# Kernel tuning notes

Measured on AMD Instinct MI355X. Metric: run time of the kernel, lower is better.

## Reference

```python
import jax, jax.numpy as jnp
import numpy as np

N_NODES = 30000
N_EDGES = 150000
N_REL = 10
IN_DIM = 256
OUT_DIM = 256


def setup_inputs() -> dict:
    key = jax.random.key(0)
    ks = jax.random.split(key, 10)
    s = 1.0 / np.sqrt(IN_DIM)  # ~nn.Linear init scale
    return {
        "x": jax.random.normal(ks[0], (N_NODES, IN_DIM), jnp.float32),
        "W_self": jax.random.uniform(ks[1], (IN_DIM, OUT_DIM), jnp.float32, -s, s),
        "b_self": jax.random.uniform(ks[2], (OUT_DIM,), jnp.float32, -s, s),
        "W_fwd": jax.random.uniform(ks[3], (N_REL, IN_DIM, OUT_DIM), jnp.float32, -s, s),
        "b_fwd": jax.random.uniform(ks[4], (N_REL, OUT_DIM), jnp.float32, -s, s),
        "W_rev": jax.random.uniform(ks[5], (N_REL, IN_DIM, OUT_DIM), jnp.float32, -s, s),
        "b_rev": jax.random.uniform(ks[6], (N_REL, OUT_DIM), jnp.float32, -s, s),
        "dep_idx": jax.random.randint(ks[7], (N_EDGES,), 0, N_NODES, jnp.int32),
        "rel_idx": jax.random.randint(ks[8], (N_EDGES,), 0, N_REL, jnp.int32),
        "gov_idx": jax.random.randint(ks[9], (N_EDGES,), 0, N_NODES, jnp.int32),
    }


def reference(x, W_self, b_self, W_fwd, b_fwd, W_rev, b_rev, dep_idx, rel_idx, gov_idx):
    # self transform for every token: [N, out]
    out = x @ W_self + b_self
    # transform all nodes by every relation weight up-front: [R, N, out]
    H_fwd = jnp.einsum("ni,rio->rno", x, W_fwd) + b_fwd[:, None, :]
    H_rev = jnp.einsum("ni,rio->rno", x, W_rev) + b_rev[:, None, :]
    # per-edge gather: forward msg uses governor feature, reverse msg uses dependent
    msg_fwd = H_fwd[rel_idx, gov_idx]  # [E, out]
    msg_rev = H_rev[rel_idx, dep_idx]  # [E, out]
    # scatter-add: forward msg -> dependent, reverse msg -> governor
    out = out.at[dep_idx].add(msg_fwd)
    out = out.at[gov_idx].add(msg_rev)
    return out
```

## Files before the change

### kernel.cpp

```cpp
#include <hip/hip_runtime.h>

#define N_NODES 30000
#define N_EDGES 150000
#define N_REL 10
#define DIM 256

#define SORT_BLOCKS 120
#define SORT_CHUNK ((N_EDGES + SORT_BLOCKS - 1) / SORT_BLOCKS)

#define SCAN_CHUNK 256
#define SCAN_BLOCKS ((N_NODES + SCAN_CHUNK - 1) / SCAN_CHUNK)

#define A_STRIDE 280

typedef __attribute__((ext_vector_type(8))) short bf16x8;
typedef __attribute__((ext_vector_type(4))) float f32x4;

__device__ __forceinline__ unsigned short f2bf(float f) {
  union { float f; unsigned int u; } v; v.f = f;
  unsigned int u = v.u;
  unsigned int r = u + 0x7fffu + ((u >> 16) & 1u);
  return (unsigned short)(r >> 16);
}


__global__ void conv_x_kernel(const float* __restrict__ x,
                              unsigned short* __restrict__ xbf) {
  int idx = blockIdx.x * blockDim.x + threadIdx.x;
  float4 v = reinterpret_cast<const float4*>(x)[idx];
  ushort4 o;
  o.x = f2bf(v.x); o.y = f2bf(v.y); o.z = f2bf(v.z); o.w = f2bf(v.w);
  reinterpret_cast<ushort4*>(xbf)[idx] = o;
}

__global__ void conv_w_kernel(const float* __restrict__ Wf,
                              const float* __restrict__ Wr,
                              const float* __restrict__ Ws,
                              unsigned short* __restrict__ wt) {
  int idx = blockIdx.x * blockDim.x + threadIdx.x;
  int b = idx >> 16;
  int t = idx & 65535;
  int o = t >> 8, i = t & 255;
  const float* src = (b < N_REL) ? (Wf + (size_t)b * 65536)
                   : (b < 2 * N_REL) ? (Wr + (size_t)(b - N_REL) * 65536)
                   : Ws;
  wt[idx] = f2bf(src[i * 256 + o]);
}

__global__ void zero_cnt_kernel(int* __restrict__ cnt, int n) {
  int i = blockIdx.x * blockDim.x + threadIdx.x;
  if (i < n) cnt[i] = 0;
}

__global__ void hist_all_kernel(const int* __restrict__ rel,
                                const int* __restrict__ dep,
                                const int* __restrict__ gov,
                                int* __restrict__ block_counts,
                                int* __restrict__ cnt) {
  __shared__ int h[N_REL];
  if (threadIdx.x < N_REL) h[threadIdx.x] = 0;
  __syncthreads();
  int beg = blockIdx.x * SORT_CHUNK;
  int end = min(beg + SORT_CHUNK, N_EDGES);
  for (int e = beg + threadIdx.x; e < end; e += blockDim.x) {
    atomicAdd(&h[rel[e]], 1);
    atomicAdd(&cnt[dep[e]], 1);
    atomicAdd(&cnt[N_NODES + gov[e]], 1);
  }
  __syncthreads();
  if (threadIdx.x < N_REL)
    block_counts[blockIdx.x * N_REL + threadIdx.x] = h[threadIdx.x];
}

__global__ void scan_rel_kernel(const int* __restrict__ block_counts,
                                int* __restrict__ rel_start,
                                int* __restrict__ block_offset) {
  __shared__ int tot[N_REL];
  int r = threadIdx.x;
  if (r < N_REL) {
    int s = 0;
    for (int b = 0; b < SORT_BLOCKS; ++b) s += block_counts[b * N_REL + r];
    tot[r] = s;
  }
  __syncthreads();
  if (threadIdx.x == 0) {
    int s = 0;
    for (int i = 0; i < N_REL; ++i) { rel_start[i] = s; s += tot[i]; }
    rel_start[N_REL] = s;
  }
  __syncthreads();
  if (r < N_REL) {
    int run = rel_start[r];
    for (int b = 0; b < SORT_BLOCKS; ++b) {
      block_offset[b * N_REL + r] = run;
      run += block_counts[b * N_REL + r];
    }
  }
}

__global__ void scanA_kernel(const int* __restrict__ cnt,
                             int* __restrict__ tmp, int* __restrict__ sums) {
  __shared__ int s[SCAN_CHUNK];
  int d = blockIdx.y, b = blockIdx.x, t = threadIdx.x;
  int i = b * SCAN_CHUNK + t;
  int v = (i < N_NODES) ? cnt[d * N_NODES + i] : 0;
  s[t] = v;
  __syncthreads();
  for (int off = 1; off < SCAN_CHUNK; off <<= 1) {
    int add = (t >= off) ? s[t - off] : 0;
    __syncthreads();
    s[t] += add;
    __syncthreads();
  }
  if (i < N_NODES) tmp[d * N_NODES + i] = s[t] - v;
  if (t == SCAN_CHUNK - 1) sums[d * SCAN_BLOCKS + b] = s[t];
}

__global__ void scanB_kernel(const int* __restrict__ sums,
                             int* __restrict__ chunk_off, int* __restrict__ rp) {
  __shared__ int s[128];
  int d = blockIdx.x, t = threadIdx.x;
  int v = (t < SCAN_BLOCKS) ? sums[d * SCAN_BLOCKS + t] : 0;
  s[t] = v;
  __syncthreads();
  for (int off = 1; off < 128; off <<= 1) {
    int add = (t >= off) ? s[t - off] : 0;
    __syncthreads();
    s[t] += add;
    __syncthreads();
  }
  if (t < SCAN_BLOCKS) chunk_off[d * SCAN_BLOCKS + t] = s[t] - v;
  if (t == 127) rp[d * (N_NODES + 1) + N_NODES] = s[127];
}

__global__ void scanC_kernel(const int* __restrict__ tmp,
                             const int* __restrict__ chunk_off,
                             int* __restrict__ rp, int* __restrict__ cursor) {
  int d = blockIdx.y;
  int i = blockIdx.x * SCAN_CHUNK + threadIdx.x;
  if (i < N_NODES) {
    int v = tmp[d * N_NODES + i] + chunk_off[d * SCAN_BLOCKS + blockIdx.x];
    rp[d * (N_NODES + 1) + i] = v;
    cursor[d * N_NODES + i] = v;
  }
}

__global__ void scatter_all_kernel(const int* __restrict__ rel,
                                   const int* __restrict__ dep,
                                   const int* __restrict__ gov,
                                   const int* __restrict__ block_offset,
                                   int* __restrict__ cursor,
                                   int* __restrict__ perm,
                                   int* __restrict__ colf,
                                   int* __restrict__ colr) {
  __shared__ int cur[N_REL];
  if (threadIdx.x < N_REL)
    cur[threadIdx.x] = block_offset[blockIdx.x * N_REL + threadIdx.x];
  __syncthreads();
  int beg = blockIdx.x * SORT_CHUNK;
  int end = min(beg + SORT_CHUNK, N_EDGES);
  for (int e = beg + threadIdx.x; e < end; e += blockDim.x) {
    int pos = atomicAdd(&cur[rel[e]], 1);
    perm[pos] = e;
    colf[atomicAdd(&cursor[dep[e]], 1)] = pos;
    colr[atomicAdd(&cursor[N_NODES + gov[e]], 1)] = pos;
  }
}


__global__ __launch_bounds__(256, 2)
void self_gemm_kernel(const unsigned short* __restrict__ xbf,
                      const unsigned short* __restrict__ wt_self,
                      const float* __restrict__ b_self,
                      float* __restrict__ out) {
  const int tid = threadIdx.x;
  const int wave = tid >> 6, lane = tid & 63;
  const int lm = lane & 15, q = lane >> 4;
  const int nb = wave * 64;

  bf16x8 wf[8][4];
  #pragma unroll
  for (int kk = 0; kk < 8; ++kk)
    #pragma unroll
    for (int ni = 0; ni < 4; ++ni)
      wf[kk][ni] = *reinterpret_cast<const bf16x8*>(
          wt_self + (size_t)(nb + ni * 16 + lm) * DIM + kk * 32 + q * 8);

  float bias[4];
  #pragma unroll
  for (int ni = 0; ni < 4; ++ni) bias[ni] = b_self[nb + ni * 16 + lm];

  const int ntiles = (N_NODES + 63) / 64;
  for (int t = blockIdx.x; t < ntiles; t += gridDim.x) {
    const int row0 = t * 64;
    const unsigned short* xr[4];
    #pragma unroll
    for (int mi = 0; mi < 4; ++mi) {
      int r = row0 + mi * 16 + lm;
      int rc = r < N_NODES ? r : N_NODES - 1;
      xr[mi] = xbf + (size_t)rc * DIM + q * 8;
    }

    f32x4 acc[4][4];
    #pragma unroll
    for (int mi = 0; mi < 4; ++mi)
      #pragma unroll
      for (int ni = 0; ni < 4; ++ni)
        acc[mi][ni] = (f32x4){0.f, 0.f, 0.f, 0.f};

    #pragma unroll
    for (int kk = 0; kk < 8; ++kk) {
      bf16x8 a[4];
      #pragma unroll
      for (int mi = 0; mi < 4; ++mi)
        a[mi] = *reinterpret_cast<const bf16x8*>(xr[mi] + kk * 32);
      #pragma unroll
      for (int mi = 0; mi < 4; ++mi)
        #pragma unroll
        for (int ni = 0; ni < 4; ++ni)
          acc[mi][ni] = __builtin_amdgcn_mfma_f32_16x16x32_bf16(a[mi], wf[kk][ni], acc[mi][ni], 0, 0, 0);
    }

    #pragma unroll
    for (int mi = 0; mi < 4; ++mi) {
      #pragma unroll
      for (int reg = 0; reg < 4; ++reg) {
        int row = row0 + mi * 16 + q * 4 + reg;
        if (row < N_NODES) {
          #pragma unroll
          for (int ni = 0; ni < 4; ++ni)
            out[(size_t)row * DIM + nb + ni * 16 + lm] = acc[mi][ni][reg] + bias[ni];
        }
      }
    }
  }
}


__global__ __launch_bounds__(256, 2)
void edge_gemm_p1_kernel(const unsigned short* __restrict__ xbf,
                         const unsigned short* __restrict__ wt,
                         const float* __restrict__ b_fwd,
                         const float* __restrict__ b_rev,
                         const int* __restrict__ perm,
                         const int* __restrict__ rel_start,
                         const int* __restrict__ dep,
                         const int* __restrict__ gov,
                         unsigned short* __restrict__ msg) {
  const int bkt = blockIdx.y;
  const int r = bkt % N_REL;
  const bool fwd = bkt < N_REL;
  const int* src_idx = fwd ? gov : dep;
  unsigned short* mdir = msg + (fwd ? 0 : (size_t)N_EDGES * DIM);
  const int beg = rel_start[r];
  const int cnt = rel_start[r + 1] - beg;
  const int ntiles = (cnt + 63) >> 6;

  const int tid = threadIdx.x;
  const int wave = tid >> 6, lane = tid & 63;
  const int lm = lane & 15, q = lane >> 4;
  const int nb = wave * 64;

  __shared__ int s_src[64];
  __shared__ unsigned short sA[64 * A_STRIDE];

  bf16x8 wf[8][4];
  const unsigned short* wbase = wt + (size_t)bkt * DIM * DIM;
  #pragma unroll
  for (int kk = 0; kk < 8; ++kk)
    #pragma unroll
    for (int ni = 0; ni < 4; ++ni)
      wf[kk][ni] = *reinterpret_cast<const bf16x8*>(
          wbase + (size_t)(nb + ni * 16 + lm) * DIM + kk * 32 + q * 8);

  const float* bptr = (fwd ? b_fwd : b_rev) + r * DIM;
  float bias[4];
  #pragma unroll
  for (int ni = 0; ni < 4; ++ni) bias[ni] = bptr[nb + ni * 16 + lm];

  for (int t = blockIdx.x; t < ntiles; t += gridDim.x) {
    const int tile0 = t << 6;
    const int rows_valid = min(64, cnt - tile0);

    if (tid < 64) {
      int s = 0;
      if (tid < rows_valid) s = src_idx[perm[beg + tile0 + tid]];
      s_src[tid] = s;
    }
    __syncthreads();

    {
      int half = lane >> 5;
      int lcol = lane & 31;
      #pragma unroll
      for (int i = 0; i < 8; ++i) {
        int row = wave * 16 + i * 2 + half;
        uint4 v = *reinterpret_cast<const uint4*>(
            xbf + (size_t)s_src[row] * DIM + lcol * 8);
        *reinterpret_cast<uint4*>(sA + row * A_STRIDE + lcol * 8) = v;
      }
    }
    __syncthreads();

    f32x4 acc[4][4];
    #pragma unroll
    for (int mi = 0; mi < 4; ++mi)
      #pragma unroll
      for (int ni = 0; ni < 4; ++ni)
        acc[mi][ni] = (f32x4){0.f, 0.f, 0.f, 0.f};

    #pragma unroll
    for (int kk = 0; kk < 8; ++kk) {
      bf16x8 a[4];
      #pragma unroll
      for (int mi = 0; mi < 4; ++mi)
        a[mi] = *reinterpret_cast<const bf16x8*>(
            sA + (mi * 16 + lm) * A_STRIDE + kk * 32 + q * 8);
      #pragma unroll
      for (int mi = 0; mi < 4; ++mi)
        #pragma unroll
        for (int ni = 0; ni < 4; ++ni)
          acc[mi][ni] = __builtin_amdgcn_mfma_f32_16x16x32_bf16(a[mi], wf[kk][ni], acc[mi][ni], 0, 0, 0);
    }
    __syncthreads();

    #pragma unroll
    for (int mi = 0; mi < 4; ++mi)
      #pragma unroll
      for (int reg = 0; reg < 4; ++reg) {
        int row = mi * 16 + q * 4 + reg;
        #pragma unroll
        for (int ni = 0; ni < 4; ++ni)
          sA[row * DIM + nb + ni * 16 + lm] = f2bf(acc[mi][ni][reg] + bias[ni]);
      }
    __syncthreads();

    unsigned short* mbase = mdir + (size_t)(beg + tile0) * DIM;
    #pragma unroll
    for (int it = 0; it < 8; ++it) {
      int elem = it * 2048 + tid * 8;
      if ((elem >> 8) < rows_valid) {
        uint4 v = *reinterpret_cast<const uint4*>(sA + elem);
        *reinterpret_cast<uint4*>(mbase + elem) = v;
      }
    }
    __syncthreads();
  }
}


__global__ void reduce_both_kernel(const unsigned short* __restrict__ msg,
                                   const int* __restrict__ rp,
                                   const int* __restrict__ colf,
                                   const int* __restrict__ colr,
                                   float* __restrict__ out) {
  const int n = blockIdx.x, t = threadIdx.x;
  const int g = t >> 6, lane = t & 63;
  const int b0 = rp[n], e0 = rp[n + 1];
  const int b1 = rp[(N_NODES + 1) + n], e1 = rp[(N_NODES + 1) + n + 1];
  if (e0 <= b0 && e1 <= b1) return;

  float a0 = 0.f, a1 = 0.f, a2 = 0.f, a3 = 0.f;
  for (int j = b0 + g; j < e0; j += 4) {
    int row = colf[j];
    uint2 v = *reinterpret_cast<const uint2*>(msg + (size_t)row * DIM + lane * 4);
    union { unsigned int u; float f; } c;
    c.u = v.x << 16;          a0 += c.f;
    c.u = v.x & 0xffff0000u;  a1 += c.f;
    c.u = v.y << 16;          a2 += c.f;
    c.u = v.y & 0xffff0000u;  a3 += c.f;
  }
  for (int j = b1 + g; j < e1; j += 4) {
    int row = colr[j];
    uint2 v = *reinterpret_cast<const uint2*>(
        msg + (size_t)(N_EDGES + row) * DIM + lane * 4);
    union { unsigned int u; float f; } c;
    c.u = v.x << 16;          a0 += c.f;
    c.u = v.x & 0xffff0000u;  a1 += c.f;
    c.u = v.y << 16;          a2 += c.f;
    c.u = v.y & 0xffff0000u;  a3 += c.f;
  }

  __shared__ float part[4][DIM];
  part[g][lane * 4 + 0] = a0;
  part[g][lane * 4 + 1] = a1;
  part[g][lane * 4 + 2] = a2;
  part[g][lane * 4 + 3] = a3;
  __syncthreads();
  float s = part[0][t] + part[1][t] + part[2][t] + part[3][t];
  out[(size_t)n * DIM + t] += s;
}


__global__ void edge_gemm_atomic_kernel(const unsigned short* __restrict__ xbf,
                                        const unsigned short* __restrict__ wt,
                                        const float* __restrict__ b_fwd,
                                        const float* __restrict__ b_rev,
                                        const int* __restrict__ perm,
                                        const int* __restrict__ rel_start,
                                        const int* __restrict__ dep,
                                        const int* __restrict__ gov,
                                        float* __restrict__ out) {
  const int bucket = blockIdx.y;
  const int r = bucket % N_REL;
  const bool fwd = bucket < N_REL;
  const int beg = rel_start[r];
  const int cnt = rel_start[r + 1] - beg;
  const int ntiles = (cnt + 63) >> 6;

  const int tid = threadIdx.x;
  const int wave = tid >> 6, lane = tid & 63;
  const int lm = lane & 15, q = lane >> 4;
  const int nb = wave * 64;

  __shared__ int s_src[64], s_dst[64];

  const unsigned short* wr[4];
  #pragma unroll
  for (int ni = 0; ni < 4; ++ni)
    wr[ni] = wt + (size_t)bucket * DIM * DIM + (size_t)(nb + ni * 16 + lm) * DIM + q * 8;

  const float* bptr = (fwd ? b_fwd : b_rev) + r * DIM;
  float bias[4];
  #pragma unroll
  for (int ni = 0; ni < 4; ++ni) bias[ni] = bptr[nb + ni * 16 + lm];

  for (int t = blockIdx.x; t < ntiles; t += gridDim.x) {
    const int tile0 = t << 6;
    const int rows_valid = min(64, cnt - tile0);

    if (tid < 64) {
      int s = 0, d = -1;
      if (tid < rows_valid) {
        int e = perm[beg + tile0 + tid];
        int gv = gov[e], dp = dep[e];
        s = fwd ? gv : dp;
        d = fwd ? dp : gv;
      }
      s_src[tid] = s;
      s_dst[tid] = d;
    }
    __syncthreads();

    const unsigned short* xr[4];
    #pragma unroll
    for (int mi = 0; mi < 4; ++mi)
      xr[mi] = xbf + (size_t)s_src[mi * 16 + lm] * DIM + q * 8;

    f32x4 acc[4][4];
    #pragma unroll
    for (int mi = 0; mi < 4; ++mi)
      #pragma unroll
      for (int ni = 0; ni < 4; ++ni)
        acc[mi][ni] = (f32x4){0.f, 0.f, 0.f, 0.f};

    #pragma unroll
    for (int k0 = 0; k0 < DIM; k0 += 32) {
      bf16x8 a[4], b[4];
      #pragma unroll
      for (int mi = 0; mi < 4; ++mi) a[mi] = *reinterpret_cast<const bf16x8*>(xr[mi] + k0);
      #pragma unroll
      for (int ni = 0; ni < 4; ++ni) b[ni] = *reinterpret_cast<const bf16x8*>(wr[ni] + k0);
      #pragma unroll
      for (int mi = 0; mi < 4; ++mi)
        #pragma unroll
        for (int ni = 0; ni < 4; ++ni)
          acc[mi][ni] = __builtin_amdgcn_mfma_f32_16x16x32_bf16(a[mi], b[ni], acc[mi][ni], 0, 0, 0);
    }

    #pragma unroll
    for (int mi = 0; mi < 4; ++mi) {
      #pragma unroll
      for (int reg = 0; reg < 4; ++reg) {
        int row = mi * 16 + q * 4 + reg;
        if (row < rows_valid) {
          int dst = s_dst[row];
          float* op = out + (size_t)dst * DIM + nb + lm;
          #pragma unroll
          for (int ni = 0; ni < 4; ++ni)
            atomicAdd(op + ni * 16, acc[mi][ni][reg] + bias[ni]);
        }
      }
    }
    __syncthreads();
  }
}


extern "C" void kernel_launch(void* const* d_in, const int* in_sizes, int n_in,
                              void* d_out, int out_size, void* d_ws, size_t ws_size,
                              hipStream_t stream) {
  const float* x      = (const float*)d_in[0];
  const float* W_self = (const float*)d_in[1];
  const float* b_self = (const float*)d_in[2];
  const float* W_fwd  = (const float*)d_in[3];
  const float* b_fwd  = (const float*)d_in[4];
  const float* W_rev  = (const float*)d_in[5];
  const float* b_rev  = (const float*)d_in[6];
  const int* dep = (const int*)d_in[7];
  const int* rel = (const int*)d_in[8];
  const int* gov = (const int*)d_in[9];
  float* out = (float*)d_out;

  char* base = (char*)d_ws;
  size_t off = 0;
  auto alloc = [&](size_t bytes) -> char* {
    char* p = base + off;
    off = (off + bytes + 15) & ~(size_t)15;
    return p;
  };

  unsigned short* xbf = (unsigned short*)alloc((size_t)N_NODES * DIM * 2);
  unsigned short* wt  = (unsigned short*)alloc((size_t)21 * DIM * DIM * 2);
  int* perm          = (int*)alloc((size_t)N_EDGES * 4);
  int* rel_start     = (int*)alloc(16 * 4);
  int* block_counts  = (int*)alloc(SORT_BLOCKS * N_REL * 4);
  int* block_offset  = (int*)alloc(SORT_BLOCKS * N_REL * 4);
  int* cnt       = (int*)alloc((size_t)2 * N_NODES * 4);
  int* tmp       = (int*)alloc((size_t)2 * N_NODES * 4);
  int* sums      = (int*)alloc((size_t)2 * SCAN_BLOCKS * 4);
  int* chunk_off = (int*)alloc((size_t)2 * SCAN_BLOCKS * 4);
  int* rp        = (int*)alloc((size_t)2 * (N_NODES + 1) * 4);
  int* cursor    = (int*)alloc((size_t)2 * N_NODES * 4);
  int* colf      = (int*)alloc((size_t)N_EDGES * 4);
  int* colr      = (int*)alloc((size_t)N_EDGES * 4);
  unsigned short* msg = (unsigned short*)alloc((size_t)2 * N_EDGES * DIM * 2);
  const bool two_phase = (off <= ws_size);

  conv_x_kernel<<<N_NODES * DIM / 4 / 256, 256, 0, stream>>>(x, xbf);
  conv_w_kernel<<<21 * DIM * DIM / 256, 256, 0, stream>>>(W_fwd, W_rev, W_self, wt);

  if (two_phase) {
    zero_cnt_kernel<<<(2 * N_NODES + 255) / 256, 256, 0, stream>>>(cnt, 2 * N_NODES);
    hist_all_kernel<<<SORT_BLOCKS, 256, 0, stream>>>(rel, dep, gov, block_counts, cnt);
    scan_rel_kernel<<<1, 64, 0, stream>>>(block_counts, rel_start, block_offset);
    scanA_kernel<<<dim3(SCAN_BLOCKS, 2), SCAN_CHUNK, 0, stream>>>(cnt, tmp, sums);
    scanB_kernel<<<2, 128, 0, stream>>>(sums, chunk_off, rp);
    scanC_kernel<<<dim3(SCAN_BLOCKS, 2), SCAN_CHUNK, 0, stream>>>(tmp, chunk_off, rp, cursor);
    scatter_all_kernel<<<SORT_BLOCKS, 256, 0, stream>>>(
        rel, dep, gov, block_offset, cursor, perm, colf, colr);

    self_gemm_kernel<<<120, 256, 0, stream>>>(
        xbf, wt + (size_t)20 * DIM * DIM, b_self, out);

    edge_gemm_p1_kernel<<<dim3(48, 2 * N_REL), 256, 0, stream>>>(
        xbf, wt, b_fwd, b_rev, perm, rel_start, dep, gov, msg);
    reduce_both_kernel<<<N_NODES, 256, 0, stream>>>(msg, rp, colf, colr, out);
  } else {
    zero_cnt_kernel<<<(2 * N_NODES + 255) / 256, 256, 0, stream>>>(cnt, 2 * N_NODES);
    hist_all_kernel<<<SORT_BLOCKS, 256, 0, stream>>>(rel, dep, gov, block_counts, cnt);
    scan_rel_kernel<<<1, 64, 0, stream>>>(block_counts, rel_start, block_offset);
    scanA_kernel<<<dim3(SCAN_BLOCKS, 2), SCAN_CHUNK, 0, stream>>>(cnt, tmp, sums);
    scanB_kernel<<<2, 128, 0, stream>>>(sums, chunk_off, rp);
    scanC_kernel<<<dim3(SCAN_BLOCKS, 2), SCAN_CHUNK, 0, stream>>>(tmp, chunk_off, rp, cursor);
    scatter_all_kernel<<<SORT_BLOCKS, 256, 0, stream>>>(
        rel, dep, gov, block_offset, cursor, perm, colf, colr);
    self_gemm_kernel<<<120, 256, 0, stream>>>(
        xbf, wt + (size_t)20 * DIM * DIM, b_self, out);
    edge_gemm_atomic_kernel<<<dim3(260, 20), 256, 0, stream>>>(
        xbf, wt, b_fwd, b_rev, perm, rel_start, dep, gov, out);
  }
}
```

Baseline: 303.0 us.

## Fuse prep kernels and merge self GEMM into edge GEMM launch

Merges the x conversion, weight transpose-conversion and counter zeroing into one prep kernel. The self-transform GEMM becomes an extra grid row of the edge GEMM kernel, so both run in one launch and share the machine. Edge messages are now written straight from registers as packed bf16 pairs, skipping the LDS staging pass and two barriers, with a matching column permutation in the reduce kernel. This trades launch overhead and tail gaps for a more complex kernel and less coalesced message stores.

```diff
diff --git a/kernel.cpp b/kernel.cpp
--- a/kernel.cpp
+++ b/kernel.cpp
@@ -12,6 +12,10 @@
 #define SCAN_BLOCKS ((N_NODES + SCAN_CHUNK - 1) / SCAN_CHUNK)
 
 #define A_STRIDE 280
+
+#define PREP_XB 7500
+#define PREP_WB 5376
+#define PREP_ZB 235
 
 typedef __attribute__((ext_vector_type(8))) short bf16x8;
 typedef __attribute__((ext_vector_type(4))) float f32x4;
@@ -24,32 +28,33 @@
 }
 
 
-__global__ void conv_x_kernel(const float* __restrict__ x,
-                              unsigned short* __restrict__ xbf) {
-  int idx = blockIdx.x * blockDim.x + threadIdx.x;
-  float4 v = reinterpret_cast<const float4*>(x)[idx];
-  ushort4 o;
-  o.x = f2bf(v.x); o.y = f2bf(v.y); o.z = f2bf(v.z); o.w = f2bf(v.w);
-  reinterpret_cast<ushort4*>(xbf)[idx] = o;
-}
-
-__global__ void conv_w_kernel(const float* __restrict__ Wf,
-                              const float* __restrict__ Wr,
-                              const float* __restrict__ Ws,
-                              unsigned short* __restrict__ wt) {
-  int idx = blockIdx.x * blockDim.x + threadIdx.x;
-  int b = idx >> 16;
-  int t = idx & 65535;
-  int o = t >> 8, i = t & 255;
-  const float* src = (b < N_REL) ? (Wf + (size_t)b * 65536)
-                   : (b < 2 * N_REL) ? (Wr + (size_t)(b - N_REL) * 65536)
-                   : Ws;
-  wt[idx] = f2bf(src[i * 256 + o]);
-}
-
-__global__ void zero_cnt_kernel(int* __restrict__ cnt, int n) {
-  int i = blockIdx.x * blockDim.x + threadIdx.x;
-  if (i < n) cnt[i] = 0;
+__global__ void prep_kernel(const float* __restrict__ x,
+                            const float* __restrict__ Wf,
+                            const float* __restrict__ Wr,
+                            const float* __restrict__ Ws,
+                            unsigned short* __restrict__ xbf,
+                            unsigned short* __restrict__ wt,
+                            int* __restrict__ cnt) {
+  int b = blockIdx.x;
+  if (b < PREP_XB) {
+    int idx = b * 256 + threadIdx.x;
+    float4 v = reinterpret_cast<const float4*>(x)[idx];
+    ushort4 o;
+    o.x = f2bf(v.x); o.y = f2bf(v.y); o.z = f2bf(v.z); o.w = f2bf(v.w);
+    reinterpret_cast<ushort4*>(xbf)[idx] = o;
+  } else if (b < PREP_XB + PREP_WB) {
+    int idx = (b - PREP_XB) * 256 + threadIdx.x;
+    int bb = idx >> 16;
+    int t = idx & 65535;
+    int o = t >> 8, i = t & 255;
+    const float* src = (bb < N_REL) ? (Wf + (size_t)bb * 65536)
+                     : (bb < 2 * N_REL) ? (Wr + (size_t)(bb - N_REL) * 65536)
+                     : Ws;
+    wt[idx] = f2bf(src[i * 256 + o]);
+  } else {
+    int i = (b - PREP_XB - PREP_WB) * 256 + threadIdx.x;
+    if (i < 2 * N_NODES) cnt[i] = 0;
+  }
 }
 
 __global__ void hist_all_kernel(const int* __restrict__ rel,
@@ -169,98 +174,34 @@
 
 
 __global__ __launch_bounds__(256, 2)
-void self_gemm_kernel(const unsigned short* __restrict__ xbf,
-                      const unsigned short* __restrict__ wt_self,
+void mega_gemm_kernel(const unsigned short* __restrict__ xbf,
+                      const unsigned short* __restrict__ wt,
                       const float* __restrict__ b_self,
+                      const float* __restrict__ b_fwd,
+                      const float* __restrict__ b_rev,
+                      const int* __restrict__ perm,
+                      const int* __restrict__ rel_start,
+                      const int* __restrict__ dep,
+                      const int* __restrict__ gov,
+                      unsigned short* __restrict__ msg,
                       float* __restrict__ out) {
+  const int bkt = blockIdx.y;
+  const bool is_self = (bkt == 2 * N_REL);
+  const int r = bkt % N_REL;
+  const bool fwd = bkt < N_REL;
+
+  int beg, cnt;
+  const int* src_idx = fwd ? gov : dep;
+  unsigned short* mdir = msg + (fwd ? 0 : (size_t)N_EDGES * DIM);
+  if (is_self) { beg = 0; cnt = N_NODES; }
+  else { beg = rel_start[r]; cnt = rel_start[r + 1] - beg; }
+  const int ntiles = (cnt + 63) >> 6;
+
   const int tid = threadIdx.x;
   const int wave = tid >> 6, lane = tid & 63;
   const int lm = lane & 15, q = lane >> 4;
   const int nb = wave * 64;
 
-  bf16x8 wf[8][4];
-  #pragma unroll
-  for (int kk = 0; kk < 8; ++kk)
-    #pragma unroll
-    for (int ni = 0; ni < 4; ++ni)
-      wf[kk][ni] = *reinterpret_cast<const bf16x8*>(
-          wt_self + (size_t)(nb + ni * 16 + lm) * DIM + kk * 32 + q * 8);
-
-  float bias[4];
-  #pragma unroll
-  for (int ni = 0; ni < 4; ++ni) bias[ni] = b_self[nb + ni * 16 + lm];
-
-  const int ntiles = (N_NODES + 63) / 64;
-  for (int t = blockIdx.x; t < ntiles; t += gridDim.x) {
-    const int row0 = t * 64;
-    const unsigned short* xr[4];
-    #pragma unroll
-    for (int mi = 0; mi < 4; ++mi) {
-      int r = row0 + mi * 16 + lm;
-      int rc = r < N_NODES ? r : N_NODES - 1;
-      xr[mi] = xbf + (size_t)rc * DIM + q * 8;
-    }
-
-    f32x4 acc[4][4];
-    #pragma unroll
-    for (int mi = 0; mi < 4; ++mi)
-      #pragma unroll
-      for (int ni = 0; ni < 4; ++ni)
-        acc[mi][ni] = (f32x4){0.f, 0.f, 0.f, 0.f};
-
-    #pragma unroll
-    for (int kk = 0; kk < 8; ++kk) {
-      bf16x8 a[4];
-      #pragma unroll
-      for (int mi = 0; mi < 4; ++mi)
-        a[mi] = *reinterpret_cast<const bf16x8*>(xr[mi] + kk * 32);
-      #pragma unroll
-      for (int mi = 0; mi < 4; ++mi)
-        #pragma unroll
-        for (int ni = 0; ni < 4; ++ni)
-          acc[mi][ni] = __builtin_amdgcn_mfma_f32_16x16x32_bf16(a[mi], wf[kk][ni], acc[mi][ni], 0, 0, 0);
-    }
-
-    #pragma unroll
-    for (int mi = 0; mi < 4; ++mi) {
-      #pragma unroll
-      for (int reg = 0; reg < 4; ++reg) {
-        int row = row0 + mi * 16 + q * 4 + reg;
-        if (row < N_NODES) {
-          #pragma unroll
-          for (int ni = 0; ni < 4; ++ni)
-            out[(size_t)row * DIM + nb + ni * 16 + lm] = acc[mi][ni][reg] + bias[ni];
-        }
-      }
-    }
-  }
-}
-
-
-__global__ __launch_bounds__(256, 2)
-void edge_gemm_p1_kernel(const unsigned short* __restrict__ xbf,
-                         const unsigned short* __restrict__ wt,
-                         const float* __restrict__ b_fwd,
-                         const float* __restrict__ b_rev,
-                         const int* __restrict__ perm,
-                         const int* __restrict__ rel_start,
-                         const int* __restrict__ dep,
-                         const int* __restrict__ gov,
-                         unsigned short* __restrict__ msg) {
-  const int bkt = blockIdx.y;
-  const int r = bkt % N_REL;
-  const bool fwd = bkt < N_REL;
-  const int* src_idx = fwd ? gov : dep;
-  unsigned short* mdir = msg + (fwd ? 0 : (size_t)N_EDGES * DIM);
-  const int beg = rel_start[r];
-  const int cnt = rel_start[r + 1] - beg;
-  const int ntiles = (cnt + 63) >> 6;
-
-  const int tid = threadIdx.x;
-  const int wave = tid >> 6, lane = tid & 63;
-  const int lm = lane & 15, q = lane >> 4;
-  const int nb = wave * 64;
-
   __shared__ int s_src[64];
   __shared__ unsigned short sA[64 * A_STRIDE];
 
@@ -273,7 +214,7 @@
       wf[kk][ni] = *reinterpret_cast<const bf16x8*>(
           wbase + (size_t)(nb + ni * 16 + lm) * DIM + kk * 32 + q * 8);
 
-  const float* bptr = (fwd ? b_fwd : b_rev) + r * DIM;
+  const float* bptr = is_self ? b_self : ((fwd ? b_fwd : b_rev) + r * DIM);
   float bias[4];
   #pragma unroll
   for (int ni = 0; ni < 4; ++ni) bias[ni] = bptr[nb + ni * 16 + lm];
@@ -283,8 +224,13 @@
     const int rows_valid = min(64, cnt - tile0);
 
     if (tid < 64) {
-      int s = 0;
-      if (tid < rows_valid) s = src_idx[perm[beg + tile0 + tid]];
+      int s;
+      if (is_self) {
+        int rr = tile0 + tid;
+        s = rr < N_NODES ? rr : N_NODES - 1;
+      } else {
+        s = (tid < rows_valid) ? src_idx[perm[beg + tile0 + tid]] : 0;
+      }
       s_src[tid] = s;
     }
     __syncthreads();
@@ -322,26 +268,37 @@
         for (int ni = 0; ni < 4; ++ni)
           acc[mi][ni] = __builtin_amdgcn_mfma_f32_16x16x32_bf16(a[mi], wf[kk][ni], acc[mi][ni], 0, 0, 0);
     }
-    __syncthreads();
-
-    #pragma unroll
-    for (int mi = 0; mi < 4; ++mi)
-      #pragma unroll
-      for (int reg = 0; reg < 4; ++reg) {
-        int row = mi * 16 + q * 4 + reg;
+
+    if (is_self) {
+      #pragma unroll
+      for (int mi = 0; mi < 4; ++mi) {
         #pragma unroll
-        for (int ni = 0; ni < 4; ++ni)
-          sA[row * DIM + nb + ni * 16 + lm] = f2bf(acc[mi][ni][reg] + bias[ni]);
-      }
-    __syncthreads();
-
-    unsigned short* mbase = mdir + (size_t)(beg + tile0) * DIM;
-    #pragma unroll
-    for (int it = 0; it < 8; ++it) {
-      int elem = it * 2048 + tid * 8;
-      if ((elem >> 8) < rows_valid) {
-        uint4 v = *reinterpret_cast<const uint4*>(sA + elem);
-        *reinterpret_cast<uint4*>(mbase + elem) = v;
+        for (int reg = 0; reg < 4; ++reg) {
+          int row = mi * 16 + q * 4 + reg;
+          if (row < rows_valid) {
+            #pragma unroll
+            for (int ni = 0; ni < 4; ++ni)
+              out[(size_t)(tile0 + row) * DIM + nb + ni * 16 + lm] =
+                  acc[mi][ni][reg] + bias[ni];
+          }
+        }
+      }
+    } else {
+      #pragma unroll
+      for (int mi = 0; mi < 4; ++mi) {
+        #pragma unroll
+        for (int reg = 0; reg < 4; ++reg) {
+          int row = mi * 16 + q * 4 + reg;
+          if (row < rows_valid) {
+            unsigned int p0 = ((unsigned int)f2bf(acc[mi][1][reg] + bias[1]) << 16) |
+                              f2bf(acc[mi][0][reg] + bias[0]);
+            unsigned int p1 = ((unsigned int)f2bf(acc[mi][3][reg] + bias[3]) << 16) |
+                              f2bf(acc[mi][2][reg] + bias[2]);
+            uint2 u; u.x = p0; u.y = p1;
+            *reinterpret_cast<uint2*>(
+                mdir + (size_t)(beg + tile0 + row) * DIM + nb + lm * 4) = u;
+          }
+        }
       }
     }
     __syncthreads();
@@ -382,15 +339,84 @@
   }
 
   __shared__ float part[4][DIM];
-  part[g][lane * 4 + 0] = a0;
-  part[g][lane * 4 + 1] = a1;
-  part[g][lane * 4 + 2] = a2;
-  part[g][lane * 4 + 3] = a3;
+  const int cb = (lane >> 4) * 64 + (lane & 15);
+  part[g][cb +  0] = a0;
+  part[g][cb + 16] = a1;
+  part[g][cb + 32] = a2;
+  part[g][cb + 48] = a3;
   __syncthreads();
   float s = part[0][t] + part[1][t] + part[2][t] + part[3][t];
   out[(size_t)n * DIM + t] += s;
 }
 
+
+__global__ __launch_bounds__(256, 2)
+void self_gemm_kernel(const unsigned short* __restrict__ xbf,
+                      const unsigned short* __restrict__ wt_self,
+                      const float* __restrict__ b_self,
+                      float* __restrict__ out) {
+  const int tid = threadIdx.x;
+  const int wave = tid >> 6, lane = tid & 63;
+  const int lm = lane & 15, q = lane >> 4;
+  const int nb = wave * 64;
+
+  bf16x8 wf[8][4];
+  #pragma unroll
+  for (int kk = 0; kk < 8; ++kk)
+    #pragma unroll
+    for (int ni = 0; ni < 4; ++ni)
+      wf[kk][ni] = *reinterpret_cast<const bf16x8*>(
+          wt_self + (size_t)(nb + ni * 16 + lm) * DIM + kk * 32 + q * 8);
+
+  float bias[4];
+  #pragma unroll
+  for (int ni = 0; ni < 4; ++ni) bias[ni] = b_self[nb + ni * 16 + lm];
+
+  const int ntiles = (N_NODES + 63) / 64;
+  for (int t = blockIdx.x; t < ntiles; t += gridDim.x) {
+    const int row0 = t * 64;
+    const unsigned short* xr[4];
+    #pragma unroll
+    for (int mi = 0; mi < 4; ++mi) {
+      int r = row0 + mi * 16 + lm;
+      int rc = r < N_NODES ? r : N_NODES - 1;
+      xr[mi] = xbf + (size_t)rc * DIM + q * 8;
+    }
+
+    f32x4 acc[4][4];
+    #pragma unroll
+    for (int mi = 0; mi < 4; ++mi)
+      #pragma unroll
+      for (int ni = 0; ni < 4; ++ni)
+        acc[mi][ni] = (f32x4){0.f, 0.f, 0.f, 0.f};
+
+    #pragma unroll
+    for (int kk = 0; kk < 8; ++kk) {
+      bf16x8 a[4];
+      #pragma unroll
+      for (int mi = 0; mi < 4; ++mi)
+        a[mi] = *reinterpret_cast<const bf16x8*>(xr[mi] + kk * 32);
+      #pragma unroll
+      for (int mi = 0; mi < 4; ++mi)
+        #pragma unroll
+        for (int ni = 0; ni < 4; ++ni)
+          acc[mi][ni] = __builtin_amdgcn_mfma_f32_16x16x32_bf16(a[mi], wf[kk][ni], acc[mi][ni], 0, 0, 0);
+    }
+
+    #pragma unroll
+    for (int mi = 0; mi < 4; ++mi) {
+      #pragma unroll
+      for (int reg = 0; reg < 4; ++reg) {
+        int row = row0 + mi * 16 + q * 4 + reg;
+        if (row < N_NODES) {
+          #pragma unroll
+          for (int ni = 0; ni < 4; ++ni)
+            out[(size_t)row * DIM + nb + ni * 16 + lm] = acc[mi][ni][reg] + bias[ni];
+        }
+      }
+    }
+  }
+}
 
 __global__ void edge_gemm_atomic_kernel(const unsigned short* __restrict__ xbf,
                                         const unsigned short* __restrict__ wt,
@@ -527,34 +553,21 @@
   unsigned short* msg = (unsigned short*)alloc((size_t)2 * N_EDGES * DIM * 2);
   const bool two_phase = (off <= ws_size);
 
-  conv_x_kernel<<<N_NODES * DIM / 4 / 256, 256, 0, stream>>>(x, xbf);
-  conv_w_kernel<<<21 * DIM * DIM / 256, 256, 0, stream>>>(W_fwd, W_rev, W_self, wt);
+  prep_kernel<<<PREP_XB + PREP_WB + PREP_ZB, 256, 0, stream>>>(
+      x, W_fwd, W_rev, W_self, xbf, wt, cnt);
+  hist_all_kernel<<<SORT_BLOCKS, 256, 0, stream>>>(rel, dep, gov, block_counts, cnt);
+  scan_rel_kernel<<<1, 64, 0, stream>>>(block_counts, rel_start, block_offset);
+  scanA_kernel<<<dim3(SCAN_BLOCKS, 2), SCAN_CHUNK, 0, stream>>>(cnt, tmp, sums);
+  scanB_kernel<<<2, 128, 0, stream>>>(sums, chunk_off, rp);
+  scanC_kernel<<<dim3(SCAN_BLOCKS, 2), SCAN_CHUNK, 0, stream>>>(tmp, chunk_off, rp, cursor);
+  scatter_all_kernel<<<SORT_BLOCKS, 256, 0, stream>>>(
+      rel, dep, gov, block_offset, cursor, perm, colf, colr);
 
   if (two_phase) {
-    zero_cnt_kernel<<<(2 * N_NODES + 255) / 256, 256, 0, stream>>>(cnt, 2 * N_NODES);
-    hist_all_kernel<<<SORT_BLOCKS, 256, 0, stream>>>(rel, dep, gov, block_counts, cnt);
-    scan_rel_kernel<<<1, 64, 0, stream>>>(block_counts, rel_start, block_offset);
-    scanA_kernel<<<dim3(SCAN_BLOCKS, 2), SCAN_CHUNK, 0, stream>>>(cnt, tmp, sums);
-    scanB_kernel<<<2, 128, 0, stream>>>(sums, chunk_off, rp);
-    scanC_kernel<<<dim3(SCAN_BLOCKS, 2), SCAN_CHUNK, 0, stream>>>(tmp, chunk_off, rp, cursor);
-    scatter_all_kernel<<<SORT_BLOCKS, 256, 0, stream>>>(
-        rel, dep, gov, block_offset, cursor, perm, colf, colr);
-
-    self_gemm_kernel<<<120, 256, 0, stream>>>(
-        xbf, wt + (size_t)20 * DIM * DIM, b_self, out);
-
-    edge_gemm_p1_kernel<<<dim3(48, 2 * N_REL), 256, 0, stream>>>(
-        xbf, wt, b_fwd, b_rev, perm, rel_start, dep, gov, msg);
+    mega_gemm_kernel<<<dim3(48, 2 * N_REL + 1), 256, 0, stream>>>(
+        xbf, wt, b_self, b_fwd, b_rev, perm, rel_start, dep, gov, msg, out);
     reduce_both_kernel<<<N_NODES, 256, 0, stream>>>(msg, rp, colf, colr, out);
   } else {
-    zero_cnt_kernel<<<(2 * N_NODES + 255) / 256, 256, 0, stream>>>(cnt, 2 * N_NODES);
-    hist_all_kernel<<<SORT_BLOCKS, 256, 0, stream>>>(rel, dep, gov, block_counts, cnt);
-    scan_rel_kernel<<<1, 64, 0, stream>>>(block_counts, rel_start, block_offset);
-    scanA_kernel<<<dim3(SCAN_BLOCKS, 2), SCAN_CHUNK, 0, stream>>>(cnt, tmp, sums);
-    scanB_kernel<<<2, 128, 0, stream>>>(sums, chunk_off, rp);
-    scanC_kernel<<<dim3(SCAN_BLOCKS, 2), SCAN_CHUNK, 0, stream>>>(tmp, chunk_off, rp, cursor);
-    scatter_all_kernel<<<SORT_BLOCKS, 256, 0, stream>>>(
-        rel, dep, gov, block_offset, cursor, perm, colf, colr);
     self_gemm_kernel<<<120, 256, 0, stream>>>(
         xbf, wt + (size_t)20 * DIM * DIM, b_self, out);
     edge_gemm_atomic_kernel<<<dim3(260, 20), 256, 0, stream>>>(
```

After: 280.9 us. 1.08x faster.
